# Kernel optimization log

Measured on AMD Instinct MI355X. Metric: run time of the kernel, lower is better.

## Reference

```python
import jax, jax.numpy as jnp
import numpy as np

N = 100000
E = 3200000
F_IN = 512
NUM_CLASSES = 8
H1, C1 = 4, 8   # conv1: 4 heads, 8 channels each (concat -> 32)
H2, C2 = 1, NUM_CLASSES  # conv2: 1 head, mean (concat=False)
NEG_SLOPE = 0.2


def gat_conv(x, W, att_src, att_dst, bias, src, dst, num_nodes, concat):
    """PyG-style GATConv (eval mode, self-loops already in src/dst)."""
    H, C = att_src.shape
    xp = (x @ W).reshape(-1, H, C)              # [N, H, C]
    a_s = (xp * att_src[None]).sum(-1)           # [N, H]
    a_d = (xp * att_dst[None]).sum(-1)           # [N, H]
    e = jax.nn.leaky_relu(a_s[src] + a_d[dst], NEG_SLOPE)  # [E, H]
    # segment softmax over destination nodes (stable)
    e_max = jax.ops.segment_max(e, dst, num_segments=num_nodes)
    e = jnp.exp(e - e_max[dst])
    denom = jax.ops.segment_sum(e, dst, num_segments=num_nodes)
    alpha = e / denom[dst]                        # [E, H]
    msg = xp[src] * alpha[..., None]              # [E, H, C]
    out = jax.ops.segment_sum(msg, dst, num_segments=num_nodes)  # [N, H, C]
    if concat:
        out = out.reshape(num_nodes, H * C)
    else:
        out = out.mean(axis=1)
    return out + bias


def setup_inputs() -> dict:
    key = jax.random.key(0)
    ks = jax.random.split(key, 9)
    s = 0.1
    return {
        "x": jax.random.normal(ks[0], (N, F_IN), dtype=jnp.float32),
        "edge_index": jax.random.randint(ks[1], (2, E), 0, N, dtype=jnp.int32),
        "W1": jax.random.normal(ks[2], (F_IN, H1 * C1), dtype=jnp.float32) * s,
        "att_src1": jax.random.normal(ks[3], (H1, C1), dtype=jnp.float32) * s,
        "att_dst1": jax.random.normal(ks[4], (H1, C1), dtype=jnp.float32) * s,
        "b1": jnp.zeros((H1 * C1,), dtype=jnp.float32),
        "W2": jax.random.normal(ks[5], (H1 * C1, H2 * C2), dtype=jnp.float32) * s,
        "att_src2": jax.random.normal(ks[6], (H2, C2), dtype=jnp.float32) * s,
        "att_dst2": jax.random.normal(ks[7], (H2, C2), dtype=jnp.float32) * s,
        "b2": jnp.zeros((C2,), dtype=jnp.float32),
    }


def reference(x, edge_index, W1, att_src1, att_dst1, b1, W2, att_src2, att_dst2, b2):
    # PyG GATConv default add_self_loops=True
    loop = jnp.arange(N, dtype=edge_index.dtype)
    src = jnp.concatenate([edge_index[0], loop])
    dst = jnp.concatenate([edge_index[1], loop])
    # dropout is identity in eval mode
    h = jax.nn.elu(gat_conv(x, W1, att_src1, att_dst1, b1, src, dst, N, True))
    out = gat_conv(h, W2, att_src2, att_dst2, b2, src, dst, N, False)
    return out
```

## Files before the change

### kernel.cpp

```cpp
#include <hip/hip_runtime.h>

typedef unsigned short u16;
typedef unsigned int   u32;

#define NN  100000
#define EE  3200000
#define ETOT 3300000
#define FIN 512
#define NBUK 512
#define NPB  196
#define CAP  8192
#define TILE_A 8192
#define NBLK_A ((ETOT + TILE_A - 1) / TILE_A)

typedef __attribute__((ext_vector_type(8))) short bfx8;
typedef __attribute__((ext_vector_type(4))) float f32x4;

__device__ __forceinline__ float bf2f(u16 u){ return __uint_as_float(((u32)u) << 16); }
__device__ __forceinline__ float lo16f(u32 v){ return __uint_as_float(v << 16); }
__device__ __forceinline__ float hi16f(u32 v){ return __uint_as_float(v & 0xffff0000u); }
__device__ __forceinline__ u16 f2bf(float f){
  u32 u = __float_as_uint(f);
  u += 0x7fffu + ((u >> 16) & 1u);
  return (u16)(u >> 16);
}
__device__ __forceinline__ u32 pack2(float a, float b){
  return ((u32)f2bf(b) << 16) | (u32)f2bf(a);
}


__global__ void __launch_bounds__(256) k_binA(const int* __restrict__ ei,
                                              u32* __restrict__ gcnt,
                                              u32* __restrict__ buk){
  __shared__ u32 hcnt[NBUK];
  __shared__ u32 hbase[NBUK];
  int t = threadIdx.x;
  hcnt[t] = 0; hcnt[t + 256] = 0;
  __syncthreads();
  int e0 = blockIdx.x * TILE_A;
  u32 pk[32], meta[32];
  #pragma unroll
  for (int i = 0; i < 32; i++){
    int e = e0 + i*256 + t;
    if (e < ETOT){
      int s, d;
      if (e < EE){ s = ei[e]; d = ei[EE + e]; } else { s = e - EE; d = s; }
      u32 b = (u32)d / NPB;
      pk[i] = ((u32)(d - (int)b*NPB) << 17) | (u32)s;
      u32 r = atomicAdd(&hcnt[b], 1u);
      meta[i] = (b << 13) | r;
    } else meta[i] = 0xFFFFFFFFu;
  }
  __syncthreads();
  for (int q = t; q < NBUK; q += 256){
    u32 c = hcnt[q];
    if (c) hbase[q] = atomicAdd(&gcnt[q], c);
  }
  __syncthreads();
  #pragma unroll
  for (int i = 0; i < 32; i++){
    if (meta[i] != 0xFFFFFFFFu){
      u32 b = meta[i] >> 13, r = meta[i] & 8191u;
      buk[((u32)b << 13) + hbase[b] + r] = pk[i];
    }
  }
}

__global__ void __launch_bounds__(512) k_bscan(const u32* __restrict__ gcnt,
                                               u32* __restrict__ sbase){
  __shared__ u32 sd[512];
  int t = threadIdx.x;
  u32 v = gcnt[t];
  sd[t] = v; __syncthreads();
  for (int o = 1; o < 512; o <<= 1){
    u32 x = (t >= o) ? sd[t - o] : 0;
    __syncthreads();
    sd[t] += x;
    __syncthreads();
  }
  sbase[t] = sd[t] - v;
}

__global__ void __launch_bounds__(256) k_scatterB(const u32* __restrict__ gcnt,
                                                  const u32* __restrict__ sbase,
                                                  const u32* __restrict__ buk,
                                                  int2* __restrict__ range,
                                                  int* __restrict__ srcs){
  __shared__ u32 dcnt[NPB + 1];
  __shared__ u32 cur[NPB];
  int b = blockIdx.x, t = threadIdx.x;
  u32 lo = (u32)b << 13;
  u32 hi = lo + gcnt[b];
  u32 gb = sbase[b];
  if (t < NPB + 1) dcnt[t] = 0;
  __syncthreads();
  for (u32 j = lo + t; j < hi; j += 256)
    atomicAdd(&dcnt[(buk[j] >> 17) + 1], 1u);
  __syncthreads();
  for (int o = 1; o < 256; o <<= 1){
    u32 x = 0;
    if (t < NPB + 1 && t >= o) x = dcnt[t - o];
    __syncthreads();
    if (t < NPB + 1 && t >= o) dcnt[t] += x;
    __syncthreads();
  }
  if (t < NPB){
    u32 beg = gb + dcnt[t];
    cur[t] = beg;
    int node = b * NPB + t;
    if (node < NN){
      u32 end = gb + dcnt[t + 1];
      range[node] = make_int2((int)beg, (int)end);
    }
  }
  __syncthreads();
  for (u32 j = lo + t; j < hi; j += 256){
    u32 p = buk[j];
    u32 pos = atomicAdd(&cur[p >> 17], 1u);
    srcs[pos] = (int)(p & 0x1FFFFu);
  }
}


__global__ void k_prep_w(const float* __restrict__ W1, u16* __restrict__ WTb){
  int i = blockIdx.x*blockDim.x + threadIdx.x;
  if (i >= FIN*32) return;
  int k = i >> 5, c = i & 31;
  WTb[c*FIN + k] = f2bf(W1[i]);
}

__global__ void __launch_bounds__(256) k_gemm1(
    const float* __restrict__ x, const u16* __restrict__ WTb,
    const float* __restrict__ attS, const float* __restrict__ attD,
    u16* __restrict__ xp1, float* __restrict__ as1, float* __restrict__ ad1){
  __shared__ u16 ws[32 * 520];
  int tid = threadIdx.x;
  int nb  = blockIdx.x * 64;

  {
    int r = tid >> 3, seg = tid & 7;
    const uint4* src = (const uint4*)(WTb + r*FIN + seg*64);
    uint4* dst = (uint4*)(ws + r*520 + seg*64);
    #pragma unroll
    for (int i = 0; i < 8; i++) dst[i] = src[i];
  }
  __syncthreads();

  int lane = tid & 63, wid = tid >> 6;
  int m = lane & 15, quad = lane >> 4;
  int rowbase = wid * 16;
  int row = nb + rowbase + m; if (row >= NN) row = NN - 1;
  const float* xrow = x + (size_t)row * FIN + quad * 8;
  const u16* b0_base = ws + m * 520 + quad * 8;
  const u16* b1_base = b0_base + 16 * 520;

  f32x4 acc0 = {0.f, 0.f, 0.f, 0.f};
  f32x4 acc1 = {0.f, 0.f, 0.f, 0.f};

  union Ubf { bfx8 v; u32 u[4]; };

  #pragma unroll
  for (int kc = 0; kc < 4; kc++){
    #pragma unroll
    for (int ks = 0; ks < 4; ks++){
      const float4* g = (const float4*)(xrow + kc*128 + ks*32);
      float4 f0 = g[0], f1 = g[1];
      Ubf ua;
      ua.u[0] = pack2(f0.x, f0.y); ua.u[1] = pack2(f0.z, f0.w);
      ua.u[2] = pack2(f1.x, f1.y); ua.u[3] = pack2(f1.z, f1.w);
      bfx8 b0 = *(const bfx8*)(b0_base + kc*128 + ks*32);
      bfx8 b1 = *(const bfx8*)(b1_base + kc*128 + ks*32);
      acc0 = __builtin_amdgcn_mfma_f32_16x16x32_bf16(ua.v, b0, acc0, 0, 0, 0);
      acc1 = __builtin_amdgcn_mfma_f32_16x16x32_bf16(ua.v, b1, acc1, 0, 0, 0);
    }
  }

  #pragma unroll
  for (int t = 0; t < 2; t++){
    f32x4 acc = t ? acc1 : acc0;
    int colg = t*16 + m;
    float aS = attS[colg], aD = attD[colg];
    #pragma unroll
    for (int r = 0; r < 4; r++){
      int node = nb + rowbase + quad*4 + r;
      float v = acc[r];
      if (node < NN) xp1[(size_t)node*32 + colg] = f2bf(v);
      float ps = v * aS, pd = v * aD;
      ps += __shfl_xor(ps, 1); ps += __shfl_xor(ps, 2); ps += __shfl_xor(ps, 4);
      pd += __shfl_xor(pd, 1); pd += __shfl_xor(pd, 2); pd += __shfl_xor(pd, 4);
      if ((m & 7) == 0 && node < NN){
        as1[node*4 + (colg >> 3)] = ps;
        ad1[node*4 + (colg >> 3)] = pd;
      }
    }
  }
}

__global__ void __launch_bounds__(256) k_agg1(
    const int2* __restrict__ range, const int* __restrict__ srcs,
    const u32* __restrict__ xp1u, const float* __restrict__ as1,
    const float* __restrict__ ad1, const float* __restrict__ b1,
    u32* __restrict__ hfeatu){
  int wid = (blockIdx.x * 256 + threadIdx.x) >> 6;
  if (wid >= NN) return;
  int lane = threadIdx.x & 63;
  int e = lane >> 4;
  int l = lane & 15;
  int h = l >> 2;
  int2 rr = range[wid];
  int beg = rr.x, end = rr.y;
  float ad = ad1[wid*4 + h];
  float num0 = 0.f, num1 = 0.f, den = 0.f;
  int j = beg + e;
  for (; j + 4 < end; j += 8){
    int s0 = srcs[j], s1 = srcs[j + 4];
    u32 v0 = xp1u[(size_t)s0*16 + l];
    u32 v1 = xp1u[(size_t)s1*16 + l];
    float z0 = as1[s0*4 + h] + ad;
    float z1 = as1[s1*4 + h] + ad;
    z0 = (z0 >= 0.f) ? z0 : 0.2f * z0;
    z1 = (z1 >= 0.f) ? z1 : 0.2f * z1;
    float w0 = __expf(z0), w1 = __expf(z1);
    num0 = fmaf(w0, lo16f(v0), num0); num1 = fmaf(w0, hi16f(v0), num1); den += w0;
    num0 = fmaf(w1, lo16f(v1), num0); num1 = fmaf(w1, hi16f(v1), num1); den += w1;
  }
  for (; j < end; j += 4){
    int s0 = srcs[j];
    u32 v0 = xp1u[(size_t)s0*16 + l];
    float z0 = as1[s0*4 + h] + ad;
    z0 = (z0 >= 0.f) ? z0 : 0.2f * z0;
    float w0 = __expf(z0);
    num0 = fmaf(w0, lo16f(v0), num0); num1 = fmaf(w0, hi16f(v0), num1); den += w0;
  }
  num0 += __shfl_xor(num0, 16); num0 += __shfl_xor(num0, 32);
  num1 += __shfl_xor(num1, 16); num1 += __shfl_xor(num1, 32);
  den  += __shfl_xor(den, 16);  den  += __shfl_xor(den, 32);
  if (e == 0){
    float o0 = num0 / den + b1[2*l];
    float o1 = num1 / den + b1[2*l + 1];
    o0 = (o0 > 0.f) ? o0 : (__expf(o0) - 1.f);
    o1 = (o1 > 0.f) ? o1 : (__expf(o1) - 1.f);
    hfeatu[(size_t)wid*16 + l] = pack2(o0, o1);
  }
}

__global__ void k_feat2(const u16* __restrict__ hfeat, const float* __restrict__ W2,
                        const float* __restrict__ attS, const float* __restrict__ attD,
                        float* __restrict__ xp2, float* __restrict__ as2,
                        float* __restrict__ ad2){
  int n = blockIdx.x*blockDim.x + threadIdx.x;
  if (n >= NN) return;
  const u16* hr = hfeat + (size_t)n*32;
  float h[32];
  #pragma unroll
  for (int k = 0; k < 32; k++) h[k] = bf2f(hr[k]);
  float o[8];
  #pragma unroll
  for (int j = 0; j < 8; j++) o[j] = 0.f;
  #pragma unroll
  for (int k = 0; k < 32; k++){
    #pragma unroll
    for (int j = 0; j < 8; j++) o[j] = fmaf(h[k], W2[k*8 + j], o[j]);
  }
  float s = 0.f, d = 0.f;
  #pragma unroll
  for (int j = 0; j < 8; j++){
    xp2[(size_t)n*8 + j] = o[j];
    s = fmaf(o[j], attS[j], s);
    d = fmaf(o[j], attD[j], d);
  }
  as2[n] = s; ad2[n] = d;
}

__global__ void __launch_bounds__(256) k_agg2(
    const int2* __restrict__ range, const int* __restrict__ srcs,
    const float* __restrict__ xp2, const float* __restrict__ as2,
    const float* __restrict__ ad2, const float* __restrict__ b2,
    float* __restrict__ out){
  int wid = (blockIdx.x * 256 + threadIdx.x) >> 6;
  if (wid >= NN) return;
  int lane = threadIdx.x & 63;
  int p = lane >> 3, c = lane & 7;
  int2 rr = range[wid];
  int beg = rr.x, end = rr.y;
  float ad = ad2[wid];
  float num = 0.f, den = 0.f;
  int j = beg + p;
  for (; j + 8 < end; j += 16){
    int s0 = srcs[j], s1 = srcs[j + 8];
    float v0 = xp2[(size_t)s0*8 + c];
    float v1 = xp2[(size_t)s1*8 + c];
    float z0 = as2[s0] + ad;
    float z1 = as2[s1] + ad;
    z0 = (z0 >= 0.f) ? z0 : 0.2f * z0;
    z1 = (z1 >= 0.f) ? z1 : 0.2f * z1;
    float w0 = __expf(z0), w1 = __expf(z1);
    num = fmaf(w0, v0, num); den += w0;
    num = fmaf(w1, v1, num); den += w1;
  }
  for (; j < end; j += 8){
    int s0 = srcs[j];
    float v0 = xp2[(size_t)s0*8 + c];
    float z0 = as2[s0] + ad;
    z0 = (z0 >= 0.f) ? z0 : 0.2f * z0;
    float w0 = __expf(z0);
    num = fmaf(w0, v0, num); den += w0;
  }
  num += __shfl_xor(num, 8);  den += __shfl_xor(den, 8);
  num += __shfl_xor(num, 16); den += __shfl_xor(den, 16);
  num += __shfl_xor(num, 32); den += __shfl_xor(den, 32);
  if (p == 0){
    out[(size_t)wid*8 + c] = num / den + b2[c];
  }
}

extern "C" void kernel_launch(void* const* d_in, const int* in_sizes, int n_in,
                              void* d_out, int out_size, void* d_ws, size_t ws_size,
                              hipStream_t stream){
  (void)in_sizes; (void)n_in; (void)out_size; (void)ws_size;
  const float* x   = (const float*)d_in[0];
  const int*   ei  = (const int*)d_in[1];
  const float* W1  = (const float*)d_in[2];
  const float* aS1 = (const float*)d_in[3];
  const float* aD1 = (const float*)d_in[4];
  const float* b1  = (const float*)d_in[5];
  const float* W2  = (const float*)d_in[6];
  const float* aS2 = (const float*)d_in[7];
  const float* aD2 = (const float*)d_in[8];
  const float* b2  = (const float*)d_in[9];
  float* out = (float*)d_out;

  char* w = (char*)d_ws;
  int2*  range  = (int2*)w;  w += (size_t)NN*8;
  int*   srcs   = (int*)w;   w += (size_t)ETOT*4;
  u16*   xp1    = (u16*)w;   w += (size_t)NN*32*2;
  float* as1    = (float*)w; w += (size_t)NN*4*4;
  float* ad1    = (float*)w; w += (size_t)NN*4*4;
  u16*   hfeat  = (u16*)w;   w += (size_t)NN*32*2;
  float* xp2    = (float*)w; w += (size_t)NN*8*4;
  float* as2    = (float*)w; w += (size_t)NN*4;
  float* ad2    = (float*)w; w += (size_t)NN*4;
  u16*   WTb    = (u16*)w;   w += 32*512*2;
  u32*   gcnt   = (u32*)w;   w += NBUK*4;
  u32*   sbase  = (u32*)w;   w += NBUK*4;
  u32*   buk    = (u32*)xp1;

  hipMemsetAsync(gcnt, 0, NBUK*4, stream);
  k_binA    <<<NBLK_A, 256, 0, stream>>>(ei, gcnt, buk);
  k_bscan   <<<1, 512, 0, stream>>>(gcnt, sbase);
  k_scatterB<<<NBUK, 256, 0, stream>>>(gcnt, sbase, buk, range, srcs);
  k_prep_w  <<<64, 256, 0, stream>>>(W1, WTb);
  k_gemm1   <<<(NN+63)/64, 256, 0, stream>>>(x, WTb, aS1, aD1, xp1, as1, ad1);
  k_agg1    <<<NN/4, 256, 0, stream>>>(range, srcs, (const u32*)xp1, as1, ad1, b1, (u32*)hfeat);
  k_feat2   <<<(NN+255)/256, 256, 0, stream>>>(hfeat, W2, aS2, aD2, xp2, as2, ad2);
  k_agg2    <<<NN/4, 256, 0, stream>>>(range, srcs, xp2, as2, ad2, b2, out);
}
```

Baseline: 506.1 us.

## Fuse edge binning and first GEMM into one launch; fold scan into scatter

Edge bucketing blocks and the x@W1 GEMM blocks now run in a single heterogeneous kernel, so the memory-bound binning and the GEMM overlap on the GPU. This only happens when the workspace is large enough to give the bucket buffer its own space instead of aliasing xp1. The separate bucket prefix-scan kernel is removed: each scatter block sums the preceding bucket counts itself. The memset is folded into the weight-prep kernel. The trade-offs are extra workspace, a shared-memory footprint set by the larger of the two roles, and redundant prefix reductions in every scatter block.

```diff
diff --git a/kernel.cpp b/kernel.cpp
--- a/kernel.cpp
+++ b/kernel.cpp
@@ -12,6 +12,7 @@
 #define CAP  8192
 #define TILE_A 8192
 #define NBLK_A ((ETOT + TILE_A - 1) / TILE_A)
+#define NBLK_G ((NN + 63) / 64)
 
 typedef __attribute__((ext_vector_type(8))) short bfx8;
 typedef __attribute__((ext_vector_type(4))) float f32x4;
@@ -28,16 +29,14 @@
   return ((u32)f2bf(b) << 16) | (u32)f2bf(a);
 }
 
-
-__global__ void __launch_bounds__(256) k_binA(const int* __restrict__ ei,
-                                              u32* __restrict__ gcnt,
-                                              u32* __restrict__ buk){
-  __shared__ u32 hcnt[NBUK];
-  __shared__ u32 hbase[NBUK];
+__device__ __forceinline__ void binA_body(int blk, const int* __restrict__ ei,
+                                          u32* __restrict__ gcnt,
+                                          u32* __restrict__ buk,
+                                          u32* hcnt, u32* hbase){
   int t = threadIdx.x;
   hcnt[t] = 0; hcnt[t + 256] = 0;
   __syncthreads();
-  int e0 = blockIdx.x * TILE_A;
+  int e0 = blk * TILE_A;
   u32 pk[32], meta[32];
   #pragma unroll
   for (int i = 0; i < 32; i++){
@@ -66,76 +65,13 @@
   }
 }
 
-__global__ void __launch_bounds__(512) k_bscan(const u32* __restrict__ gcnt,
-                                               u32* __restrict__ sbase){
-  __shared__ u32 sd[512];
-  int t = threadIdx.x;
-  u32 v = gcnt[t];
-  sd[t] = v; __syncthreads();
-  for (int o = 1; o < 512; o <<= 1){
-    u32 x = (t >= o) ? sd[t - o] : 0;
-    __syncthreads();
-    sd[t] += x;
-    __syncthreads();
-  }
-  sbase[t] = sd[t] - v;
-}
-
-__global__ void __launch_bounds__(256) k_scatterB(const u32* __restrict__ gcnt,
-                                                  const u32* __restrict__ sbase,
-                                                  const u32* __restrict__ buk,
-                                                  int2* __restrict__ range,
-                                                  int* __restrict__ srcs){
-  __shared__ u32 dcnt[NPB + 1];
-  __shared__ u32 cur[NPB];
-  int b = blockIdx.x, t = threadIdx.x;
-  u32 lo = (u32)b << 13;
-  u32 hi = lo + gcnt[b];
-  u32 gb = sbase[b];
-  if (t < NPB + 1) dcnt[t] = 0;
-  __syncthreads();
-  for (u32 j = lo + t; j < hi; j += 256)
-    atomicAdd(&dcnt[(buk[j] >> 17) + 1], 1u);
-  __syncthreads();
-  for (int o = 1; o < 256; o <<= 1){
-    u32 x = 0;
-    if (t < NPB + 1 && t >= o) x = dcnt[t - o];
-    __syncthreads();
-    if (t < NPB + 1 && t >= o) dcnt[t] += x;
-    __syncthreads();
-  }
-  if (t < NPB){
-    u32 beg = gb + dcnt[t];
-    cur[t] = beg;
-    int node = b * NPB + t;
-    if (node < NN){
-      u32 end = gb + dcnt[t + 1];
-      range[node] = make_int2((int)beg, (int)end);
-    }
-  }
-  __syncthreads();
-  for (u32 j = lo + t; j < hi; j += 256){
-    u32 p = buk[j];
-    u32 pos = atomicAdd(&cur[p >> 17], 1u);
-    srcs[pos] = (int)(p & 0x1FFFFu);
-  }
-}
-
-
-__global__ void k_prep_w(const float* __restrict__ W1, u16* __restrict__ WTb){
-  int i = blockIdx.x*blockDim.x + threadIdx.x;
-  if (i >= FIN*32) return;
-  int k = i >> 5, c = i & 31;
-  WTb[c*FIN + k] = f2bf(W1[i]);
-}
-
-__global__ void __launch_bounds__(256) k_gemm1(
+__device__ __forceinline__ void gemm_body(int gb,
     const float* __restrict__ x, const u16* __restrict__ WTb,
     const float* __restrict__ attS, const float* __restrict__ attD,
-    u16* __restrict__ xp1, float* __restrict__ as1, float* __restrict__ ad1){
-  __shared__ u16 ws[32 * 520];
+    u16* __restrict__ xp1, float* __restrict__ as1, float* __restrict__ ad1,
+    u16* ws){
   int tid = threadIdx.x;
-  int nb  = blockIdx.x * 64;
+  int nb  = gb * 64;
 
   {
     int r = tid >> 3, seg = tid & 7;
@@ -194,6 +130,89 @@
       }
     }
   }
+}
+
+
+__global__ void __launch_bounds__(256) k_fat(const int* __restrict__ ei,
+    u32* __restrict__ gcnt, u32* __restrict__ buk,
+    const float* __restrict__ x, const u16* __restrict__ WTb,
+    const float* __restrict__ attS, const float* __restrict__ attD,
+    u16* __restrict__ xp1, float* __restrict__ as1, float* __restrict__ ad1){
+  __shared__ __align__(16) char sm[32 * 520 * 2];
+  if (blockIdx.x < NBLK_A)
+    binA_body(blockIdx.x, ei, gcnt, buk, (u32*)sm, (u32*)sm + NBUK);
+  else
+    gemm_body(blockIdx.x - NBLK_A, x, WTb, attS, attD, xp1, as1, ad1, (u16*)sm);
+}
+
+__global__ void __launch_bounds__(256) k_binA(const int* __restrict__ ei,
+                                              u32* __restrict__ gcnt,
+                                              u32* __restrict__ buk){
+  __shared__ u32 sm2[NBUK*2];
+  binA_body(blockIdx.x, ei, gcnt, buk, sm2, sm2 + NBUK);
+}
+
+__global__ void __launch_bounds__(256) k_gemm1(
+    const float* __restrict__ x, const u16* __restrict__ WTb,
+    const float* __restrict__ attS, const float* __restrict__ attD,
+    u16* __restrict__ xp1, float* __restrict__ as1, float* __restrict__ ad1){
+  __shared__ u16 ws[32 * 520];
+  gemm_body(blockIdx.x, x, WTb, attS, attD, xp1, as1, ad1, ws);
+}
+
+__global__ void __launch_bounds__(256) k_scatterB(const u32* __restrict__ gcnt,
+                                                  const u32* __restrict__ buk,
+                                                  int2* __restrict__ range,
+                                                  int* __restrict__ srcs){
+  __shared__ u32 dcnt[NPB + 1];
+  __shared__ u32 cur[NPB];
+  __shared__ u32 red[256];
+  int b = blockIdx.x, t = threadIdx.x;
+  u32 acc = 0;
+  for (int i = t; i < b; i += 256) acc += gcnt[i];
+  red[t] = acc;
+  if (t < NPB + 1) dcnt[t] = 0;
+  __syncthreads();
+  for (int o = 128; o > 0; o >>= 1){
+    if (t < o) red[t] += red[t + o];
+    __syncthreads();
+  }
+  u32 gb = red[0];
+  u32 lo = (u32)b << 13;
+  u32 hi = lo + gcnt[b];
+  for (u32 j = lo + t; j < hi; j += 256)
+    atomicAdd(&dcnt[(buk[j] >> 17) + 1], 1u);
+  __syncthreads();
+  for (int o = 1; o < 256; o <<= 1){
+    u32 x = 0;
+    if (t < NPB + 1 && t >= o) x = dcnt[t - o];
+    __syncthreads();
+    if (t < NPB + 1 && t >= o) dcnt[t] += x;
+    __syncthreads();
+  }
+  if (t < NPB){
+    u32 beg = gb + dcnt[t];
+    cur[t] = beg;
+    int node = b * NPB + t;
+    if (node < NN){
+      range[node] = make_int2((int)beg, (int)(gb + dcnt[t + 1]));
+    }
+  }
+  __syncthreads();
+  for (u32 j = lo + t; j < hi; j += 256){
+    u32 p = buk[j];
+    u32 pos = atomicAdd(&cur[p >> 17], 1u);
+    srcs[pos] = (int)(p & 0x1FFFFu);
+  }
+}
+
+__global__ void k_prep_w(const float* __restrict__ W1, u16* __restrict__ WTb,
+                         u32* __restrict__ gcnt){
+  int i = blockIdx.x*blockDim.x + threadIdx.x;
+  if (i < NBUK) gcnt[i] = 0;
+  if (i >= FIN*32) return;
+  int k = i >> 5, c = i & 31;
+  WTb[c*FIN + k] = f2bf(W1[i]);
 }
 
 __global__ void __launch_bounds__(256) k_agg1(
@@ -317,7 +336,7 @@
 extern "C" void kernel_launch(void* const* d_in, const int* in_sizes, int n_in,
                               void* d_out, int out_size, void* d_ws, size_t ws_size,
                               hipStream_t stream){
-  (void)in_sizes; (void)n_in; (void)out_size; (void)ws_size;
+  (void)in_sizes; (void)n_in; (void)out_size;
   const float* x   = (const float*)d_in[0];
   const int*   ei  = (const int*)d_in[1];
   const float* W1  = (const float*)d_in[2];
@@ -331,26 +350,42 @@
   float* out = (float*)d_out;
 
   char* w = (char*)d_ws;
-  int2*  range  = (int2*)w;  w += (size_t)NN*8;
-  int*   srcs   = (int*)w;   w += (size_t)ETOT*4;
-  u16*   xp1    = (u16*)w;   w += (size_t)NN*32*2;
-  float* as1    = (float*)w; w += (size_t)NN*4*4;
-  float* ad1    = (float*)w; w += (size_t)NN*4*4;
-  u16*   hfeat  = (u16*)w;   w += (size_t)NN*32*2;
-  float* xp2    = (float*)w; w += (size_t)NN*8*4;
-  float* as2    = (float*)w; w += (size_t)NN*4;
-  float* ad2    = (float*)w; w += (size_t)NN*4;
-  u16*   WTb    = (u16*)w;   w += 32*512*2;
-  u32*   gcnt   = (u32*)w;   w += NBUK*4;
-  u32*   sbase  = (u32*)w;   w += NBUK*4;
-  u32*   buk    = (u32*)xp1;
-
-  hipMemsetAsync(gcnt, 0, NBUK*4, stream);
-  k_binA    <<<NBLK_A, 256, 0, stream>>>(ei, gcnt, buk);
-  k_bscan   <<<1, 512, 0, stream>>>(gcnt, sbase);
-  k_scatterB<<<NBUK, 256, 0, stream>>>(gcnt, sbase, buk, range, srcs);
-  k_prep_w  <<<64, 256, 0, stream>>>(W1, WTb);
-  k_gemm1   <<<(NN+63)/64, 256, 0, stream>>>(x, WTb, aS1, aD1, xp1, as1, ad1);
+  auto alloc = [&](size_t bytes) -> char* {
+    char* p = w; w += (bytes + 15) & ~(size_t)15; return p;
+  };
+
+  int2*  range  = (int2*)alloc((size_t)NN*8);
+  int*   srcs   = (int*)alloc((size_t)ETOT*4);
+  u16*   xp1    = (u16*)alloc((size_t)NN*64);
+  float* as1    = (float*)alloc((size_t)NN*16);
+  float* ad1    = (float*)alloc((size_t)NN*16);
+  u16*   hfeat  = (u16*)alloc((size_t)NN*64);
+  float* xp2    = (float*)alloc((size_t)NN*32);
+  float* as2    = (float*)alloc((size_t)NN*4);
+  float* ad2    = (float*)alloc((size_t)NN*4);
+  u16*   WTb    = (u16*)alloc(32*512*2);
+  u32*   gcnt   = (u32*)alloc(NBUK*4);
+  size_t base_need = (size_t)(w - (char*)d_ws);
+  size_t buk_bytes = (size_t)NBUK * CAP * 4;
+  bool overlap = (ws_size >= base_need + buk_bytes);
+
+  u32* buk;
+  if (overlap){
+    buk = (u32*)alloc(buk_bytes);
+  } else {
+    buk = (u32*)xp1;
+  }
+
+  k_prep_w  <<<64, 256, 0, stream>>>(W1, WTb, gcnt);
+  if (overlap){
+    k_fat   <<<NBLK_A + NBLK_G, 256, 0, stream>>>(ei, gcnt, buk, x, WTb, aS1, aD1,
+                                                  xp1, as1, ad1);
+    k_scatterB<<<NBUK, 256, 0, stream>>>(gcnt, buk, range, srcs);
+  } else {
+    k_binA  <<<NBLK_A, 256, 0, stream>>>(ei, gcnt, buk);
+    k_scatterB<<<NBUK, 256, 0, stream>>>(gcnt, buk, range, srcs);
+    k_gemm1 <<<NBLK_G, 256, 0, stream>>>(x, WTb, aS1, aD1, xp1, as1, ad1);
+  }
   k_agg1    <<<NN/4, 256, 0, stream>>>(range, srcs, (const u32*)xp1, as1, ad1, b1, (u32*)hfeat);
   k_feat2   <<<(NN+255)/256, 256, 0, stream>>>(hfeat, W2, aS2, aD2, xp2, as2, ad2);
   k_agg2    <<<NN/4, 256, 0, stream>>>(range, srcs, xp2, as2, ad2, b2, out);
```

Measured after the change: 487.2 us. 3.7% less time.
